# Kernel tuning notes

Measured on AMD Instinct MI355X. Metric: run time of the kernel, lower is better.

## Reference

```python
import jax, jax.numpy as jnp
import numpy as np

B, N, DIM, HEADS = 8, 512, 512, 16
MAX_DIST, NG = 128, 32
RBF_STOP = 20.0
EPS = 1e-5


def _ln(x, g, b):
    m = jnp.mean(x, axis=-1, keepdims=True)
    v = jnp.mean((x - m) ** 2, axis=-1, keepdims=True)
    return (x - m) * jax.lax.rsqrt(v + EPS) * g + b


def setup_inputs() -> dict:
    key = jax.random.key(0)
    ks = jax.random.split(key, 12)
    d = DIM
    s = 0.02
    return {
        "x": jax.random.normal(ks[0], (B * N, d), jnp.float32),
        "dist_matrix": jax.random.randint(ks[1], (B, N, N), 0, MAX_DIST, jnp.int32),
        "dist_3d": jax.random.uniform(ks[2], (B, N, N), jnp.float32) * RBF_STOP,
        "norm1_g": jnp.ones((d,), jnp.float32),
        "norm1_b": jnp.zeros((d,), jnp.float32),
        "in_proj_w": jax.random.normal(ks[3], (3 * d, d), jnp.float32) * s,
        "in_proj_b": jnp.zeros((3 * d,), jnp.float32),
        "out_proj_w": jax.random.normal(ks[4], (d, d), jnp.float32) * s,
        "out_proj_b": jnp.zeros((d,), jnp.float32),
        "dist_emb": jax.random.normal(ks[5], (MAX_DIST, HEADS), jnp.float32) * s,
        "rbf_w": jax.random.normal(ks[6], (HEADS, NG), jnp.float32) * s,
        "rbf_b": jnp.zeros((HEADS,), jnp.float32),
        "norm2_g": jnp.ones((d,), jnp.float32),
        "norm2_b": jnp.zeros((d,), jnp.float32),
        "ffn_w1": jax.random.normal(ks[7], (4 * d, d), jnp.float32) * s,
        "ffn_b1": jnp.zeros((4 * d,), jnp.float32),
        "ffn_w2": jax.random.normal(ks[8], (d, 4 * d), jnp.float32) * s,
        "ffn_b2": jnp.zeros((d,), jnp.float32),
        "batch": jnp.repeat(jnp.arange(B, dtype=jnp.int32), N),
    }


def reference(x, dist_matrix, dist_3d, norm1_g, norm1_b, in_proj_w, in_proj_b,
              out_proj_w, out_proj_b, dist_emb, rbf_w, rbf_b, norm2_g, norm2_b,
              ffn_w1, ffn_b1, ffn_w2, ffn_b2, batch):
    b, n = dist_matrix.shape[0], dist_matrix.shape[1]
    d = x.shape[-1]
    dh = d // HEADS
    # equal-size graphs -> to_dense_batch is a reshape, mask all-true
    xd = x.reshape(b, n, d)

    # additive attention bias: shortest-path-distance embedding + RBF projection
    dc = jnp.clip(dist_matrix, 0, MAX_DIST - 1)
    bias_spd = dist_emb[dc]                                  # [b, n, n, H]
    offset = jnp.linspace(0.0, RBF_STOP, NG, dtype=jnp.float32)
    coeff = -0.5 / (RBF_STOP / (NG - 1)) ** 2
    rbf = jnp.exp(coeff * (dist_3d[..., None] - offset) ** 2)  # [b, n, n, NG]
    bias_3d = rbf @ rbf_w.T + rbf_b                          # [b, n, n, H]
    bias = jnp.transpose(bias_spd + bias_3d, (0, 3, 1, 2))   # [b, H, n, n]

    # multi-head attention (pre-norm residual, as in source)
    h = _ln(xd, norm1_g, norm1_b)
    qkv = h @ in_proj_w.T + in_proj_b
    q, k, v = jnp.split(qkv, 3, axis=-1)
    q = q.reshape(b, n, HEADS, dh).transpose(0, 2, 1, 3)
    k = k.reshape(b, n, HEADS, dh).transpose(0, 2, 1, 3)
    v = v.reshape(b, n, HEADS, dh).transpose(0, 2, 1, 3)
    scores = jnp.einsum('bhqd,bhkd->bhqk', q, k) / jnp.sqrt(jnp.float32(dh)) + bias
    attn = jax.nn.softmax(scores, axis=-1)
    ctx = jnp.einsum('bhqk,bhkd->bhqd', attn, v)
    ctx = ctx.transpose(0, 2, 1, 3).reshape(b, n, d)
    attn_out = ctx @ out_proj_w.T + out_proj_b
    h = h + attn_out

    # FFN (dropout inactive at eval)
    h2 = _ln(h, norm2_g, norm2_b)
    ff = jax.nn.gelu(h2 @ ffn_w1.T + ffn_b1, approximate=False) @ ffn_w2.T + ffn_b2
    h = h + ff
    return h.reshape(b * n, d)
```

## Files before the change

kernel.cpp:

```cpp
#include <hip/hip_runtime.h>
#include <hip/hip_bf16.h>
#include <math.h>

#define BB 8
#define NN 512
#define DD 512
#define NH 16
#define DH 32
#define TD 1536
#define NG 32
#define MAXD 128

typedef __attribute__((ext_vector_type(8))) short bf16x8;
typedef __attribute__((ext_vector_type(4))) float f32x4;

__device__ inline short f2bf(float x) {
    __hip_bfloat16 h = __float2bfloat16(x);
    return *reinterpret_cast<short*>(&h);
}
__device__ inline float bf2f(short x) {
    union { unsigned u; float f; } c;
    c.u = ((unsigned)(unsigned short)x) << 16;
    return c.f;
}

__device__ inline void gld_lds16(const void* g, void* l) {
    __builtin_amdgcn_global_load_lds(
        (const __attribute__((address_space(1))) unsigned int*)g,
        (__attribute__((address_space(3))) unsigned int*)l, 16, 0, 0);
}

__global__ __launch_bounds__(256) void cvt_weights(
    const float* __restrict__ s0, const float* __restrict__ s1,
    const float* __restrict__ s2, const float* __restrict__ s3,
    short* __restrict__ d0, short* __restrict__ d1,
    short* __restrict__ d2, short* __restrict__ d3,
    const float* __restrict__ rbfw, const float* __restrict__ rbfb,
    short* __restrict__ Tg,
    int n0, int n1, int n2, int n3) {
    if (blockIdx.y == 4) {
        if (blockIdx.x != 0) return;
        const float STEP  = 20.0f / 31.0f;
        const float COEFF = -0.5f / (STEP * STEP);
        for (int idx = threadIdx.x; idx < 130 * 16; idx += 256) {
            const int i = idx >> 4, h = idx & 15;
            const float x = fminf((float)i, 128.0f) * (20.0f / 128.0f);
            float acc = rbfb[h];
#pragma unroll
            for (int g = 0; g < NG; g++) {
                const float t = x - (float)g * STEP;
                acc += __expf(COEFF * t * t) * rbfw[h * NG + g];
            }
            Tg[idx] = f2bf(acc);
        }
        return;
    }
    const float* s; short* d; int n;
    switch (blockIdx.y) {
        case 0: s = s0; d = d0; n = n0; break;
        case 1: s = s1; d = d1; n = n1; break;
        case 2: s = s2; d = d2; n = n2; break;
        default: s = s3; d = d3; n = n3; break;
    }
    const int i = (blockIdx.x * 256 + threadIdx.x) * 4;
    if (i >= n) return;
    const float4 v = *(const float4*)(s + i);
    short4 o;
    o.x = f2bf(v.x); o.y = f2bf(v.y); o.z = f2bf(v.z); o.w = f2bf(v.w);
    *(short4*)(d + i) = o;
}

__global__ __launch_bounds__(256) void ln_kernel(const float* __restrict__ x,
                                                 const float* __restrict__ g,
                                                 const float* __restrict__ b,
                                                 short* __restrict__ out_bf,
                                                 float* __restrict__ out_f) {
    const int row = blockIdx.x;
    const int tid = threadIdx.x;
    const int wave = tid >> 6, lane = tid & 63;
    const float* xr = x + (size_t)row * DD;
    const float v0 = xr[tid], v1 = xr[tid + 256];
    float s = v0 + v1, q = v0 * v0 + v1 * v1;
#pragma unroll
    for (int m = 1; m < 64; m <<= 1) { s += __shfl_xor(s, m); q += __shfl_xor(q, m); }
    __shared__ float ps[8];
    if (lane == 0) { ps[wave] = s; ps[wave + 4] = q; }
    __syncthreads();
    s = ps[0] + ps[1] + ps[2] + ps[3];
    q = ps[4] + ps[5] + ps[6] + ps[7];
    const float mean = s * (1.0f / DD);
    const float var  = q * (1.0f / DD) - mean * mean;
    const float rs   = rsqrtf(var + 1e-5f);
    const float o0 = (v0 - mean) * rs * g[tid] + b[tid];
    const float o1 = (v1 - mean) * rs * g[tid + 256] + b[tid + 256];
    out_bf[(size_t)row * DD + tid]       = f2bf(o0);
    out_bf[(size_t)row * DD + tid + 256] = f2bf(o1);
    if (out_f) {
        out_f[(size_t)row * DD + tid]       = o0;
        out_f[(size_t)row * DD + tid + 256] = o1;
    }
}

template <int TM, bool GELU, bool RES, int OUT>
__global__ __launch_bounds__(256) void gemm_bf16(
    const short* __restrict__ A, const short* __restrict__ Bw,
    const float* __restrict__ bias, const float* __restrict__ res,
    void* __restrict__ Cout, int M, int Nout, int K) {
    const int MI = TM / 32;
    const int bm = blockIdx.y * TM;
    const int bn = blockIdx.x * 128;
    const int tid  = threadIdx.x;
    const int wave = tid >> 6;
    const int lane = tid & 63;
    const int l16  = lane & 15;
    const int quad = lane >> 4;
    const int wr = (wave >> 1) * (TM / 2);
    const int wc = (wave & 1) * 64;

    __shared__ short As[2][TM * 32];
    __shared__ short Bs[2][128 * 32];

    f32x4 acc[MI][4];
#pragma unroll
    for (int i = 0; i < MI; i++)
#pragma unroll
        for (int j = 0; j < 4; j++) acc[i][j] = (f32x4){0.f, 0.f, 0.f, 0.f};

    auto stage = [&](int buf, int k0) {
        const short* Ab = A + (size_t)bm * K + k0;
        const short* Bb = Bw + (size_t)bn * K + k0;
#pragma unroll
        for (int j = 0; j < TM / 64; j++) {
            const int idx = j * 256 + wave * 64 + lane;
            gld_lds16(Ab + (size_t)(idx >> 2) * K + (idx & 3) * 8,
                      &As[buf][(size_t)(j * 256 + wave * 64) * 8]);
        }
#pragma unroll
        for (int j = 0; j < 2; j++) {
            const int idx = j * 256 + wave * 64 + lane;
            gld_lds16(Bb + (size_t)(idx >> 2) * K + (idx & 3) * 8,
                      &Bs[buf][(size_t)(j * 256 + wave * 64) * 8]);
        }
    };
    auto compute = [&](int buf) {
        bf16x8 af[MI], bfr[4];
#pragma unroll
        for (int i = 0; i < MI; i++)
            af[i] = *(const bf16x8*)&As[buf][(wr + i * 16 + l16) * 32 + quad * 8];
#pragma unroll
        for (int j = 0; j < 4; j++)
            bfr[j] = *(const bf16x8*)&Bs[buf][(wc + j * 16 + l16) * 32 + quad * 8];
#pragma unroll
        for (int i = 0; i < MI; i++)
#pragma unroll
            for (int j = 0; j < 4; j++)
                acc[i][j] = __builtin_amdgcn_mfma_f32_16x16x32_bf16(af[i], bfr[j], acc[i][j], 0, 0, 0);
    };

    stage(0, 0);
    __syncthreads();
    int cur = 0;
    for (int k0 = 32; k0 < K; k0 += 32) {
        stage(cur ^ 1, k0);
        compute(cur);
        __syncthreads();
        cur ^= 1;
    }
    compute(cur);

#pragma unroll
    for (int i = 0; i < MI; i++) {
#pragma unroll
        for (int r = 0; r < 4; r++) {
            const int row = bm + wr + i * 16 + quad * 4 + r;
#pragma unroll
            for (int j = 0; j < 4; j++) {
                const int col = bn + wc + j * 16 + l16;
                float v = acc[i][j][r] + bias[col];
                if (GELU) v = 0.5f * v * (1.0f + erff(v * 0.70710678118654752f));
                if (RES)  v += res[(size_t)row * Nout + col];
                if (OUT == 1) ((short*)Cout)[(size_t)row * Nout + col] = f2bf(v);
                else          ((float*)Cout)[(size_t)row * Nout + col] = v;
            }
        }
    }
}

__global__ __launch_bounds__(512) void attn_mfma(
    const short* __restrict__ qkv,
    const int* __restrict__ dist,
    const float* __restrict__ dist3d,
    const float* __restrict__ demb,
    const short* __restrict__ Tg,
    float* __restrict__ O_part,
    float* __restrict__ l_part)
{
    const int blk  = blockIdx.x;
    const int b    = blk & 7;
    const int t3   = blk >> 3;
    const int part = t3 % 3;
    const int q0   = (t3 / 3) * 16;
    const int tid  = threadIdx.x;
    const int wave = tid >> 6;
    const int lane = tid & 63;
    const int l16  = lane & 15;
    const int quad = lane >> 4;

    __shared__ short Kc[NH * 16 * 32];
    __shared__ short Vc[NH * 16 * 32];
    __shared__ short Pb[8 * 16 * 34];
    __shared__ short Tt[130 * 18];
    __shared__ short Db[128 * 18];

    for (int i = tid; i < 8 * 16 * 34; i += 512) Pb[i] = 0;
    for (int i = tid; i < 130 * 16; i += 512) Tt[(i >> 4) * 18 + (i & 15)] = Tg[i];
    for (int i = tid; i < 128 * 16; i += 512) Db[(i >> 4) * 18 + (i & 15)] = f2bf(demb[i]);

    const float scale = 0.17677669529663687f;
    bf16x8 qf[2];
#pragma unroll
    for (int h = 0; h < 2; h++) {
        const int hh = wave * 2 + h;
        qf[h] = *(const bf16x8*)(qkv + (size_t)(b * NN + q0 + l16) * TD + hh * DH + quad * 8);
    }

    f32x4 O[2][2];
    float lsum[2][4];
#pragma unroll
    for (int h = 0; h < 2; h++) {
#pragma unroll
        for (int tt = 0; tt < 2; tt++) O[h][tt] = (f32x4){0.f, 0.f, 0.f, 0.f};
#pragma unroll
        for (int r = 0; r < 4; r++) lsum[h][r] = 0.f;
    }

    const int cbeg = part * 11;
    const int cend = (part == 2) ? 32 : cbeg + 11;

    for (int c = cbeg; c < cend; c++) {
        const int k0 = c * 16;
        __syncthreads();
#pragma unroll
        for (int l = 0; l < 4; l++) {
            const int idxb = l * 512 + wave * 64;
            const int idx  = idxb + lane;
            const int kk2  = idx & 1023;
            const int h = kk2 >> 6, k = (kk2 >> 2) & 15, c4 = kk2 & 3;
            const short* src = qkv + (size_t)(b * NN + k0 + k) * TD +
                               DD * (1 + (l >> 1)) + h * 32 + c4 * 8;
            short* dstb = (l < 2 ? (short*)Kc : (short*)Vc) + (size_t)(idxb & 1023) * 8;
            gld_lds16(src, dstb);
        }
        float biasr[2][4];
        {
            const int hh0 = wave * 2, hh1 = hh0 + 1;
#pragma unroll
            for (int r = 0; r < 4; r++) {
                const size_t off = ((size_t)(b * NN) + q0 + quad * 4 + r) * NN + k0 + l16;
                int dc = dist[off];
                dc = min(max(dc, 0), MAXD - 1);
                const float x = dist3d[off] * 6.4f;
                int ii = (int)x; ii = min(ii, 127);
                const float fr = x - (float)ii;
                const float t00 = bf2f(Tt[ii * 18 + hh0]), t01 = bf2f(Tt[ii * 18 + 18 + hh0]);
                const float t10 = bf2f(Tt[ii * 18 + hh1]), t11 = bf2f(Tt[ii * 18 + 18 + hh1]);
                biasr[0][r] = bf2f(Db[dc * 18 + hh0]) + t00 + (t01 - t00) * fr;
                biasr[1][r] = bf2f(Db[dc * 18 + hh1]) + t10 + (t11 - t10) * fr;
            }
        }
        __syncthreads();
#pragma unroll
        for (int h = 0; h < 2; h++) {
            const int hh = wave * 2 + h;
            const bf16x8 kf = *(const bf16x8*)&Kc[hh * 512 + l16 * 32 + quad * 8];
            f32x4 s = __builtin_amdgcn_mfma_f32_16x16x32_bf16(
                qf[h], kf, (f32x4){0.f, 0.f, 0.f, 0.f}, 0, 0, 0);
            float pv[4];
#pragma unroll
            for (int r = 0; r < 4; r++) {
                float sv = s[r] * scale + biasr[h][r];
                sv = fminf(sv, 20.f);
                pv[r] = __expf(sv);
                lsum[h][r] += pv[r];
                Pb[wave * 544 + (quad * 4 + r) * 34 + l16] = f2bf(pv[r]);
            }
            const bf16x8 pf = *(const bf16x8*)&Pb[wave * 544 + l16 * 34 + quad * 8];
#pragma unroll
            for (int tt = 0; tt < 2; tt++) {
                bf16x8 vf;
                if (quad < 2) {
#pragma unroll
                    for (int j = 0; j < 8; j++)
                        vf[j] = Vc[hh * 512 + (quad * 8 + j) * 32 + tt * 16 + l16];
                } else {
#pragma unroll
                    for (int j = 0; j < 8; j++) vf[j] = 0;
                }
                O[h][tt] = __builtin_amdgcn_mfma_f32_16x16x32_bf16(pf, vf, O[h][tt], 0, 0, 0);
            }
        }
    }
    const size_t poff = (size_t)part * 4096;
#pragma unroll
    for (int h = 0; h < 2; h++) {
        const int hh = wave * 2 + h;
#pragma unroll
        for (int m = 1; m < 16; m <<= 1)
#pragma unroll
            for (int r = 0; r < 4; r++) lsum[h][r] += __shfl_xor(lsum[h][r], m);
#pragma unroll
        for (int r = 0; r < 4; r++) {
            const size_t row = (size_t)(b * NN + q0 + quad * 4 + r);
#pragma unroll
            for (int tt = 0; tt < 2; tt++)
                O_part[(poff + row) * DD + hh * DH + tt * 16 + l16] = O[h][tt][r];
            if (l16 == 0) l_part[(poff + row) * NH + hh] = lsum[h][r];
        }
    }
}

__global__ __launch_bounds__(256) void attn_combine(
    const float* __restrict__ O_part, const float* __restrict__ l_part,
    short* __restrict__ ctx) {
    const int e = (blockIdx.x * 256 + threadIdx.x) * 4;
    const int row = e >> 9, d = e & 511, h = d >> 5;
    const size_t PO = (size_t)4096 * 512;
    const float4 o0 = *(const float4*)(O_part + e);
    const float4 o1 = *(const float4*)(O_part + PO + e);
    const float4 o2 = *(const float4*)(O_part + 2 * PO + e);
    const int li = row * NH + h;
    const float l = l_part[li] + l_part[4096 * NH + li] + l_part[2 * 4096 * NH + li];
    const float rinv = 1.0f / l;
    short4 o;
    o.x = f2bf((o0.x + o1.x + o2.x) * rinv);
    o.y = f2bf((o0.y + o1.y + o2.y) * rinv);
    o.z = f2bf((o0.z + o1.z + o2.z) * rinv);
    o.w = f2bf((o0.w + o1.w + o2.w) * rinv);
    *(short4*)(ctx + e) = o;
}

extern "C" void kernel_launch(void* const* d_in, const int* in_sizes, int n_in,
                              void* d_out, int out_size, void* d_ws, size_t ws_size,
                              hipStream_t stream) {
    const float* x      = (const float*)d_in[0];
    const int*   dist   = (const int*)d_in[1];
    const float* dist3d = (const float*)d_in[2];
    const float* n1g    = (const float*)d_in[3];
    const float* n1b    = (const float*)d_in[4];
    const float* win    = (const float*)d_in[5];
    const float* bin    = (const float*)d_in[6];
    const float* wo     = (const float*)d_in[7];
    const float* bo     = (const float*)d_in[8];
    const float* demb   = (const float*)d_in[9];
    const float* rbfw   = (const float*)d_in[10];
    const float* rbfb   = (const float*)d_in[11];
    const float* n2g    = (const float*)d_in[12];
    const float* n2b    = (const float*)d_in[13];
    const float* w1     = (const float*)d_in[14];
    const float* b1     = (const float*)d_in[15];
    const float* w2     = (const float*)d_in[16];
    const float* b2     = (const float*)d_in[17];

    char* p = (char*)d_ws;
    short* h_bf   = (short*)p; p += (size_t)4096 * 512 * 2;
    float* h_f    = (float*)p; p += (size_t)4096 * 512 * 4;
    short* qkv_bf = (short*)p; p += (size_t)4096 * 1536 * 2;
    short* ctx_bf = (short*)p; p += (size_t)4096 * 512 * 2;
    float* hres   = (float*)p; p += (size_t)4096 * 512 * 4;
    short* h2_bf  = (short*)p; p += (size_t)4096 * 512 * 2;
    short* win_bf = (short*)p; p += (size_t)1536 * 512 * 2;
    short* wo_bf  = (short*)p; p += (size_t)512 * 512 * 2;
    short* w1_bf  = (short*)p; p += (size_t)2048 * 512 * 2;
    short* w2_bf  = (short*)p; p += (size_t)512 * 2048 * 2;
    short* Tg     = (short*)p; p += (size_t)8192;
    float* O_part = (float*)p;
    short* mid_bf = (short*)p;
    p += (size_t)3 * 4096 * 512 * 4;
    float* l_part = (float*)p; p += (size_t)3 * 4096 * 16 * 4;

    const int M = BB * NN;

    cvt_weights<<<dim3(1024, 5), 256, 0, stream>>>(
        win, wo, w1, w2, win_bf, wo_bf, w1_bf, w2_bf, rbfw, rbfb, Tg,
        1536 * 512, 512 * 512, 2048 * 512, 512 * 2048);
    ln_kernel<<<M, 256, 0, stream>>>(x, n1g, n1b, h_bf, h_f);
    gemm_bf16<64, false, false, 1><<<dim3(12, 64), 256, 0, stream>>>(
        h_bf, win_bf, bin, nullptr, qkv_bf, M, TD, DD);
    attn_mfma<<<768, 512, 0, stream>>>(
        qkv_bf, dist, dist3d, demb, Tg, O_part, l_part);
    attn_combine<<<2048, 256, 0, stream>>>(O_part, l_part, ctx_bf);
    gemm_bf16<64, false, true, 0><<<dim3(4, 64), 256, 0, stream>>>(
        ctx_bf, wo_bf, bo, h_f, hres, M, DD, DD);
    ln_kernel<<<M, 256, 0, stream>>>(hres, n2g, n2b, h2_bf, nullptr);
    gemm_bf16<64, true, false, 1><<<dim3(16, 64), 256, 0, stream>>>(
        h2_bf, w1_bf, b1, nullptr, mid_bf, M, 2048, DD);
    gemm_bf16<64, false, true, 0><<<dim3(4, 64), 256, 0, stream>>>(
        mid_bf, w2_bf, b2, hres, (float*)d_out, M, DD, 2048);
}
```

Measured before the change: 262.2 us.

## Split-K the FFN down-projection, enlarge GEMM M-tiles, and unpad the attention P buffer

The FFN second GEMM (K=2048) is split into three K-slices along blockIdx.z. Each slice writes fp32 partials, and a new combine kernel sums them and adds bias and residual. The QKV and FFN-up GEMMs move from 64-row to 128-row tiles, halving grid rows to raise reuse per block. The attention P staging buffer drops its padding from 34 to 32 columns, which shrinks LDS use but may bring bank conflicts. Split-K adds a partial-buffer write and read plus an extra launch, and it aliases the partials onto the no-longer-needed h_bf/qkv region.

Result: no change. 262.0 us (-0.1%).

```diff
diff --git a/kernel.cpp b/kernel.cpp
--- a/kernel.cpp
+++ b/kernel.cpp
@@ -101,7 +101,7 @@
     }
 }
 
-template <int TM, bool GELU, bool RES, int OUT>
+template <int TM, bool GELU, bool RES, int OUT, int SPLIT>
 __global__ __launch_bounds__(256) void gemm_bf16(
     const short* __restrict__ A, const short* __restrict__ Bw,
     const float* __restrict__ bias, const float* __restrict__ res,
@@ -117,6 +117,14 @@
     const int wr = (wave >> 1) * (TM / 2);
     const int wc = (wave & 1) * 64;
 
+    int kbeg = 0, kend = K;
+    if (SPLIT > 1) {
+        const int z = blockIdx.z;
+        const int step = (K / SPLIT) & ~31;
+        kbeg = z * step;
+        kend = (z == SPLIT - 1) ? K : kbeg + step;
+    }
+
     __shared__ short As[2][TM * 32];
     __shared__ short Bs[2][128 * 32];
 
@@ -157,10 +165,10 @@
                 acc[i][j] = __builtin_amdgcn_mfma_f32_16x16x32_bf16(af[i], bfr[j], acc[i][j], 0, 0, 0);
     };
 
-    stage(0, 0);
+    stage(0, kbeg);
     __syncthreads();
     int cur = 0;
-    for (int k0 = 32; k0 < K; k0 += 32) {
+    for (int k0 = kbeg + 32; k0 < kend; k0 += 32) {
         stage(cur ^ 1, k0);
         compute(cur);
         __syncthreads();
@@ -176,14 +184,38 @@
 #pragma unroll
             for (int j = 0; j < 4; j++) {
                 const int col = bn + wc + j * 16 + l16;
-                float v = acc[i][j][r] + bias[col];
-                if (GELU) v = 0.5f * v * (1.0f + erff(v * 0.70710678118654752f));
-                if (RES)  v += res[(size_t)row * Nout + col];
-                if (OUT == 1) ((short*)Cout)[(size_t)row * Nout + col] = f2bf(v);
-                else          ((float*)Cout)[(size_t)row * Nout + col] = v;
+                if (OUT == 2) {
+                    ((float*)Cout)[(size_t)blockIdx.z * M * Nout +
+                                   (size_t)row * Nout + col] = acc[i][j][r];
+                } else {
+                    float v = acc[i][j][r] + bias[col];
+                    if (GELU) v = 0.5f * v * (1.0f + erff(v * 0.70710678118654752f));
+                    if (RES)  v += res[(size_t)row * Nout + col];
+                    if (OUT == 1) ((short*)Cout)[(size_t)row * Nout + col] = f2bf(v);
+                    else          ((float*)Cout)[(size_t)row * Nout + col] = v;
+                }
             }
         }
     }
+}
+
+__global__ __launch_bounds__(256) void ffn2_combine(
+    const float* __restrict__ part, const float* __restrict__ bias,
+    const float* __restrict__ res, float* __restrict__ out) {
+    const int e = (blockIdx.x * 256 + threadIdx.x) * 4;
+    const int col = e & 511;
+    const size_t PO = (size_t)4096 * 512;
+    const float4 p0 = *(const float4*)(part + e);
+    const float4 p1 = *(const float4*)(part + PO + e);
+    const float4 p2 = *(const float4*)(part + 2 * PO + e);
+    const float4 rr = *(const float4*)(res + e);
+    const float4 bb = *(const float4*)(bias + col);
+    float4 o;
+    o.x = p0.x + p1.x + p2.x + bb.x + rr.x;
+    o.y = p0.y + p1.y + p2.y + bb.y + rr.y;
+    o.z = p0.z + p1.z + p2.z + bb.z + rr.z;
+    o.w = p0.w + p1.w + p2.w + bb.w + rr.w;
+    *(float4*)(out + e) = o;
 }
 
 __global__ __launch_bounds__(512) void attn_mfma(
@@ -208,11 +240,11 @@
 
     __shared__ short Kc[NH * 16 * 32];
     __shared__ short Vc[NH * 16 * 32];
-    __shared__ short Pb[8 * 16 * 34];
+    __shared__ short Pb[8 * 16 * 32];
     __shared__ short Tt[130 * 18];
     __shared__ short Db[128 * 18];
 
-    for (int i = tid; i < 8 * 16 * 34; i += 512) Pb[i] = 0;
+    for (int i = tid; i < 8 * 16 * 32; i += 512) Pb[i] = 0;
     for (int i = tid; i < 130 * 16; i += 512) Tt[(i >> 4) * 18 + (i & 15)] = Tg[i];
     for (int i = tid; i < 128 * 16; i += 512) Db[(i >> 4) * 18 + (i & 15)] = f2bf(demb[i]);
 
@@ -282,9 +314,9 @@
                 sv = fminf(sv, 20.f);
                 pv[r] = __expf(sv);
                 lsum[h][r] += pv[r];
-                Pb[wave * 544 + (quad * 4 + r) * 34 + l16] = f2bf(pv[r]);
+                Pb[wave * 512 + (quad * 4 + r) * 32 + l16] = f2bf(pv[r]);
             }
-            const bf16x8 pf = *(const bf16x8*)&Pb[wave * 544 + l16 * 34 + quad * 8];
+            const bf16x8 pf = *(const bf16x8*)&Pb[wave * 512 + l16 * 32 + quad * 8];
 #pragma unroll
             for (int tt = 0; tt < 2; tt++) {
                 bf16x8 vf;
@@ -365,6 +397,7 @@
     short* h_bf   = (short*)p; p += (size_t)4096 * 512 * 2;
     float* h_f    = (float*)p; p += (size_t)4096 * 512 * 4;
     short* qkv_bf = (short*)p; p += (size_t)4096 * 1536 * 2;
+    float* f2part = (float*)h_bf;
     short* ctx_bf = (short*)p; p += (size_t)4096 * 512 * 2;
     float* hres   = (float*)p; p += (size_t)4096 * 512 * 4;
     short* h2_bf  = (short*)p; p += (size_t)4096 * 512 * 2;
@@ -384,16 +417,17 @@
         win, wo, w1, w2, win_bf, wo_bf, w1_bf, w2_bf, rbfw, rbfb, Tg,
         1536 * 512, 512 * 512, 2048 * 512, 512 * 2048);
     ln_kernel<<<M, 256, 0, stream>>>(x, n1g, n1b, h_bf, h_f);
-    gemm_bf16<64, false, false, 1><<<dim3(12, 64), 256, 0, stream>>>(
+    gemm_bf16<128, false, false, 1, 1><<<dim3(12, 32), 256, 0, stream>>>(
         h_bf, win_bf, bin, nullptr, qkv_bf, M, TD, DD);
     attn_mfma<<<768, 512, 0, stream>>>(
         qkv_bf, dist, dist3d, demb, Tg, O_part, l_part);
     attn_combine<<<2048, 256, 0, stream>>>(O_part, l_part, ctx_bf);
-    gemm_bf16<64, false, true, 0><<<dim3(4, 64), 256, 0, stream>>>(
+    gemm_bf16<64, false, true, 0, 1><<<dim3(4, 64), 256, 0, stream>>>(
         ctx_bf, wo_bf, bo, h_f, hres, M, DD, DD);
     ln_kernel<<<M, 256, 0, stream>>>(hres, n2g, n2b, h2_bf, nullptr);
-    gemm_bf16<64, true, false, 1><<<dim3(16, 64), 256, 0, stream>>>(
+    gemm_bf16<128, true, false, 1, 1><<<dim3(16, 32), 256, 0, stream>>>(
         h2_bf, w1_bf, b1, nullptr, mid_bf, M, 2048, DD);
-    gemm_bf16<64, false, true, 0><<<dim3(4, 64), 256, 0, stream>>>(
-        mid_bf, w2_bf, b2, hres, (float*)d_out, M, DD, 2048);
-}
+    gemm_bf16<128, false, false, 2, 3><<<dim3(4, 32, 3), 256, 0, stream>>>(
+        mid_bf, w2_bf, b2, nullptr, f2part, M, DD, 2048);
+    ffn2_combine<<<2048, 256, 0, stream>>>(f2part, b2, hres, (float*)d_out);
+}
```
